# Optimization experiments

Measured on AMD Instinct MI355X. Metric: run time of the kernel, lower is better.

The kernel has to match this reference:

```python
import jax, jax.numpy as jnp
import numpy as np

EMB = 128
SQRT_EMB = 128 ** 0.5
LOGIT_CLIP = 10.0


def setup_inputs() -> dict:
    key = jax.random.key(0)
    ks = jax.random.split(key, 10)
    B, N, M, D = 128, 512, 512, EMB
    s = 1.0 / np.sqrt(D)
    return {
        "encoded_last_node": jax.random.normal(ks[0], (B, N, D), jnp.float32),
        "load": jax.random.uniform(ks[1], (B, N), jnp.float32),
        "cur_dist": jax.random.uniform(ks[2], (B, N, M), jnp.float32),
        "log_scale": jnp.ones((), jnp.float32),
        "ninf_mask": jnp.zeros((B, N, M), jnp.float32),
        "encoded_nodes": jax.random.normal(ks[3], (B, M, D), jnp.float32),
        "Wq_last": jax.random.normal(ks[4], (D, D + 1), jnp.float32) * s,
        "Wk": jax.random.normal(ks[5], (D, D), jnp.float32) * s,
        "Wv": jax.random.normal(ks[6], (D, D), jnp.float32) * s,
        "alpha1": jnp.ones((1,), jnp.float32),
        "alpha2": jnp.ones((1,), jnp.float32),
    }


def reference(encoded_last_node, load, cur_dist, log_scale, ninf_mask,
              encoded_nodes, Wq_last, Wk, Wv, alpha1, alpha2):
    # set_kv
    k = jnp.einsum('bmd,ed->bme', encoded_nodes, Wk)   # (B,M,D)
    v = jnp.einsum('bmd,ed->bme', encoded_nodes, Wv)   # (B,M,D)
    # query from last node + load
    input_cat = jnp.concatenate([encoded_last_node, load[:, :, None]], axis=2)  # (B,N,D+1)
    q = jnp.einsum('bnc,ec->bne', input_cat, Wq_last)  # (B,N,D)
    # AAFM: exp-bias linear attention with sigmoid gate
    adaptation_bias = -alpha1[0] * log_scale * cur_dist + ninf_mask  # (B,N,M)
    eb = jnp.exp(adaptation_bias)
    ek = jnp.exp(k)
    num = jnp.einsum('bnm,bmd->bnd', eb, ek * v)
    den = jnp.einsum('bnm,bmd->bnd', eb, ek)
    weighted = jnp.nan_to_num(num / den)  # mirrors torch nan_to_num correction
    aafm_out = jax.nn.sigmoid(q) * weighted  # (B,N,D)
    # single-head decode score against encoder embeddings
    score = jnp.einsum('bnd,bmd->bnm', aafm_out, encoded_nodes)
    score_scaled = score / SQRT_EMB - alpha2[0] * log_scale * cur_dist
    score_masked = LOGIT_CLIP * jnp.tanh(score_scaled) + ninf_mask
    probs = jax.nn.softmax(score_masked, axis=-1)
    return probs
```

## Files before the change

### kernel.cpp

```cpp
#include <hip/hip_runtime.h>
#include <math.h>

#define B 128
#define N 512
#define M 512
#define D 128

typedef __attribute__((ext_vector_type(8))) short s16x8;
typedef __attribute__((ext_vector_type(4))) short s16x4;
typedef __attribute__((ext_vector_type(4))) float f32x4;

#define MFMA16(a, b, c) __builtin_amdgcn_mfma_f32_16x16x32_bf16(a, b, c, 0, 0, 0)

#define FENCE()   asm volatile("" ::: "memory")
#define VMCNT4()  asm volatile("s_waitcnt vmcnt(4)" ::: "memory")
#define VMCNT8()  asm volatile("s_waitcnt vmcnt(8)" ::: "memory")
#define VMCNT12() asm volatile("s_waitcnt vmcnt(12)" ::: "memory")
#define VMCNT16() asm volatile("s_waitcnt vmcnt(16)" ::: "memory")
#define VMCNT20() asm volatile("s_waitcnt vmcnt(20)" ::: "memory")
#define LGKMCNT0() asm volatile("s_waitcnt lgkmcnt(0)" ::: "memory")
#define SCHEDBAR() __builtin_amdgcn_sched_barrier(0)

__device__ __forceinline__ void gload16(const void* g, void* l) {
    __builtin_amdgcn_global_load_lds(
        (const __attribute__((address_space(1))) unsigned int*)g,
        (__attribute__((address_space(3))) unsigned int*)l, 16, 0, 0);
}

__device__ __forceinline__ float fast_tanh(float x) {
    x = fminf(fmaxf(x, -15.f), 15.f);
    float E = __expf(2.f * x);
    return 1.f - 2.f / (E + 1.f);
}

__device__ __forceinline__ unsigned short bf16rne(float x) {
    unsigned u = __float_as_uint(x);
    return (unsigned short)((u + 0x7FFF + ((u >> 16) & 1)) >> 16);
}

__device__ __forceinline__ void fsplit(float x, short& h, short& l) {
    unsigned u = __float_as_uint(x);
    h = (short)(u >> 16);
    float fh = __uint_as_float(u & 0xffff0000u);
    l = (short)(__float_as_uint(x - fh) >> 16);
}

__device__ __forceinline__ void fsplit8(float4 x0, float4 x1, s16x8& h, s16x8& l) {
    short a, b;
    fsplit(x0.x, a, b); h[0] = a; l[0] = b;
    fsplit(x0.y, a, b); h[1] = a; l[1] = b;
    fsplit(x0.z, a, b); h[2] = a; l[2] = b;
    fsplit(x0.w, a, b); h[3] = a; l[3] = b;
    fsplit(x1.x, a, b); h[4] = a; l[4] = b;
    fsplit(x1.y, a, b); h[5] = a; l[5] = b;
    fsplit(x1.z, a, b); h[6] = a; l[6] = b;
    fsplit(x1.w, a, b); h[7] = a; l[7] = b;
}

__device__ __forceinline__ void ebpack(float4 c0, float4 c1, float4 f0, float4 f1,
                                       float a1ls, s16x8& a) {
    a[0] = (short)bf16rne(__expf(fmaf(-a1ls, c0.x, f0.x)));
    a[1] = (short)bf16rne(__expf(fmaf(-a1ls, c0.y, f0.y)));
    a[2] = (short)bf16rne(__expf(fmaf(-a1ls, c0.z, f0.z)));
    a[3] = (short)bf16rne(__expf(fmaf(-a1ls, c0.w, f0.w)));
    a[4] = (short)bf16rne(__expf(fmaf(-a1ls, c1.x, f1.x)));
    a[5] = (short)bf16rne(__expf(fmaf(-a1ls, c1.y, f1.y)));
    a[6] = (short)bf16rne(__expf(fmaf(-a1ls, c1.z, f1.z)));
    a[7] = (short)bf16rne(__expf(fmaf(-a1ls, c1.w, f1.w)));
}

__global__ void k_prep_w(const float* __restrict__ Wk, const float* __restrict__ Wv,
                         const float* __restrict__ Wq,
                         unsigned short* __restrict__ Wk_hi, unsigned short* __restrict__ Wk_lo,
                         unsigned short* __restrict__ Wv_hi, unsigned short* __restrict__ Wv_lo,
                         unsigned short* __restrict__ Wq_hi, unsigned short* __restrict__ Wq_lo) {
    int i = blockIdx.x * 256 + threadIdx.x;
    short h, l;
    if (i < 16384) {
        fsplit(Wk[i], h, l); Wk_hi[i] = (unsigned short)h; Wk_lo[i] = (unsigned short)l;
    } else if (i < 32768) {
        int j = i - 16384;
        fsplit(Wv[j], h, l); Wv_hi[j] = (unsigned short)h; Wv_lo[j] = (unsigned short)l;
    } else {
        int j = i - 32768; int e = j >> 7, d = j & 127;
        fsplit(Wq[e * 129 + d], h, l); Wq_hi[j] = (unsigned short)h; Wq_lo[j] = (unsigned short)l;
    }
}

__global__ __launch_bounds__(256) void k_kv(const float* __restrict__ enc,
        const unsigned short* __restrict__ Wk_hi, const unsigned short* __restrict__ Wk_lo,
        const unsigned short* __restrict__ Wv_hi, const unsigned short* __restrict__ Wv_lo,
        unsigned short* __restrict__ EKb, unsigned short* __restrict__ EKVb) {
    int b = blockIdx.y;
    int wave = threadIdx.x >> 6, lane = threadIdx.x & 63;
    int row = lane & 15, kg = lane >> 4;
    int m0 = blockIdx.x * 64 + wave * 16;
    f32x4 acc[16];
#pragma unroll
    for (int i = 0; i < 16; i++) acc[i] = (f32x4)0.f;
    const float* ap = enc + ((size_t)b * M + m0 + row) * D + kg * 8;
#pragma unroll
    for (int ks = 0; ks < 4; ks++) {
        float4 x0 = *(const float4*)(ap + ks * 32);
        float4 x1 = *(const float4*)(ap + ks * 32 + 4);
        s16x8 ah, al;
        fsplit8(x0, x1, ah, al);
        int wb = ks * 32 + kg * 8;
#pragma unroll
        for (int ct = 0; ct < 8; ct++) {
            int e = ct * 16 + row;
            s16x8 bh = *(const s16x8*)(Wk_hi + e * D + wb);
            s16x8 bl = *(const s16x8*)(Wk_lo + e * D + wb);
            acc[ct] = MFMA16(ah, bh, acc[ct]);
            acc[ct] = MFMA16(al, bh, acc[ct]);
            acc[ct] = MFMA16(ah, bl, acc[ct]);
            bh = *(const s16x8*)(Wv_hi + e * D + wb);
            bl = *(const s16x8*)(Wv_lo + e * D + wb);
            acc[8 + ct] = MFMA16(ah, bh, acc[8 + ct]);
            acc[8 + ct] = MFMA16(al, bh, acc[8 + ct]);
            acc[8 + ct] = MFMA16(ah, bl, acc[8 + ct]);
        }
    }
#pragma unroll
    for (int ct = 0; ct < 8; ct++) {
        int e = ct * 16 + row;
        s16x4 kb, vb;
#pragma unroll
        for (int r = 0; r < 4; r++) {
            float ek = __expf(acc[ct][r]);
            float ev = ek * acc[8 + ct][r];
            kb[r] = (short)bf16rne(ek);
            vb[r] = (short)bf16rne(ev);
        }
        int m = m0 + kg * 4;
        int chunk = (m & 31) >> 3;
        int p = chunk ^ (e & 3);
        size_t o = ((size_t)b * D + e) * M + (size_t)(m & ~31) + p * 8 + (m & 7);
        *(s16x4*)(EKb + o) = kb;
        *(s16x4*)(EKVb + o) = vb;
    }
}

__global__ void k_encpack(const float* __restrict__ enc, unsigned short* __restrict__ Eb) {
    size_t i = (size_t)blockIdx.x * 256 + threadIdx.x;
    size_t bm = i >> 4;
    int c = (int)(i & 15);
    int m = (int)(bm & 511);
    int p = c ^ (m & 7);
    const float* src = enc + bm * 128 + c * 8;
    float4 x0 = *(const float4*)(src);
    float4 x1 = *(const float4*)(src + 4);
    s16x8 v;
    v[0] = (short)bf16rne(x0.x); v[1] = (short)bf16rne(x0.y);
    v[2] = (short)bf16rne(x0.z); v[3] = (short)bf16rne(x0.w);
    v[4] = (short)bf16rne(x1.x); v[5] = (short)bf16rne(x1.y);
    v[6] = (short)bf16rne(x1.z); v[7] = (short)bf16rne(x1.w);
    *(s16x8*)(Eb + bm * 128 + p * 8) = v;
}

__global__ __launch_bounds__(256, 3) void k_fused(
        const float* __restrict__ encl, const float* __restrict__ loadv,
        const float* __restrict__ Wq,
        const unsigned short* __restrict__ Wq_hi, const unsigned short* __restrict__ Wq_lo,
        const float* __restrict__ cd, const float* __restrict__ ninf,
        const unsigned short* __restrict__ EKVb, const unsigned short* __restrict__ EKb,
        const unsigned short* __restrict__ Eb,
        const float* __restrict__ a1p, const float* __restrict__ a2p,
        const float* __restrict__ lsp, float* __restrict__ out) {
    int o = blockIdx.x;
    int xcd = o & 7, j = o >> 3;
    int b = ((j >> 4) << 3) + xcd;
    int nb = j & 15;
    int n0 = nb * 32;
    int w = threadIdx.x >> 6, lane = threadIdx.x & 63;
    int row = lane & 15, kg = lane >> 4;
    __shared__ __align__(16) char lds[32768];
    float* redm = (float*)lds;
    float* reds = (float*)(lds + 512);
    float a1ls = a1p[0] * lsp[0];
    float a2ls = a2p[0] * lsp[0];
    const float invs = 0.08838834764831845f;
    char* wb = lds + w * 8192;

    f32x4 sqa[2][2];
#pragma unroll
    for (int s = 0; s < 2; s++)
#pragma unroll
        for (int ct = 0; ct < 2; ct++) sqa[s][ct] = (f32x4)0.f;
#pragma unroll
    for (int s = 0; s < 2; s++) {
        const float* ap = encl + ((size_t)b * N + n0 + s * 16 + row) * D + kg * 8;
#pragma unroll
        for (int ks = 0; ks < 4; ks++) {
            float4 x0 = *(const float4*)(ap + ks * 32);
            float4 x1 = *(const float4*)(ap + ks * 32 + 4);
            s16x8 ah, al;
            fsplit8(x0, x1, ah, al);
            int wqo = ks * 32 + kg * 8;
#pragma unroll
            for (int ct = 0; ct < 2; ct++) {
                int e = w * 32 + ct * 16 + row;
                s16x8 bh = *(const s16x8*)(Wq_hi + e * D + wqo);
                s16x8 bl = *(const s16x8*)(Wq_lo + e * D + wqo);
                sqa[s][ct] = MFMA16(ah, bh, sqa[s][ct]);
                sqa[s][ct] = MFMA16(al, bh, sqa[s][ct]);
                sqa[s][ct] = MFMA16(ah, bl, sqa[s][ct]);
            }
        }
    }
    float sqv[2][2][4];
#pragma unroll
    for (int s = 0; s < 2; s++)
#pragma unroll
        for (int ct = 0; ct < 2; ct++) {
            int e = w * 32 + ct * 16 + row;
            float wcol = Wq[e * 129 + 128];
#pragma unroll
            for (int r = 0; r < 4; r++) {
                int n = n0 + s * 16 + kg * 4 + r;
                float q = sqa[s][ct][r] + loadv[(size_t)b * N + n] * wcol;
                sqv[s][ct][r] = 1.f / (1.f + __expf(-q));
            }
        }
    FENCE();

    f32x4 accN[2][2], accD[2][2];
#pragma unroll
    for (int s = 0; s < 2; s++)
#pragma unroll
        for (int i = 0; i < 2; i++) { accN[s][i] = (f32x4)0.f; accD[s][i] = (f32x4)0.f; }
    const char* gEKV = (const char*)EKVb + (size_t)b * D * M * 2;
    const char* gEK  = (const char*)EKb  + (size_t)b * D * M * 2;
    const float* cdp0 = cd + ((size_t)b * N + n0 + row) * M + kg * 8;
    const float* nfp0 = ninf + ((size_t)b * N + n0 + row) * M + kg * 8;
    const float* cdp1 = cdp0 + (size_t)16 * M;
    const float* nfp1 = nfp0 + (size_t)16 * M;

#define STAGE_B(bufptr, mt)                                                      \
    _Pragma("unroll")                                                            \
    for (int jv = 0; jv < 4; jv++) {                                             \
        int arr = jv >> 1;                                                       \
        int rem = (jv & 1) * 64 + lane;                                          \
        const char* gb = arr ? gEK : gEKV;                                       \
        gload16(gb + (size_t)(w * 32 + (rem >> 2)) * 1024 + (size_t)(mt) * 64 +  \
                    (rem & 3) * 16,                                              \
                (char*)(bufptr) + arr * 2048 + rem * 16);                        \
    }

    float4 Ac[2][2][2], Af[2][2][2];
#define LOAD_A(p, mt)                                                            \
    Ac[p][0][0] = *(const float4*)(cdp0 + (mt) * 32);                            \
    Ac[p][0][1] = *(const float4*)(cdp0 + (mt) * 32 + 4);                        \
    Af[p][0][0] = *(const float4*)(nfp0 + (mt) * 32);                            \
    Af[p][0][1] = *(const float4*)(nfp0 + (mt) * 32 + 4);                        \
    Ac[p][1][0] = *(const float4*)(cdp1 + (mt) * 32);                            \
    Ac[p][1][1] = *(const float4*)(cdp1 + (mt) * 32 + 4);                        \
    Af[p][1][0] = *(const float4*)(nfp1 + (mt) * 32);                            \
    Af[p][1][1] = *(const float4*)(nfp1 + (mt) * 32 + 4);

    LOAD_A(0, 0) FENCE();
    STAGE_B(wb, 0) FENCE();
    LOAD_A(1, 1) FENCE();
    STAGE_B(wb + 4096, 1) FENCE();

    int rbB = row * 64 + ((kg ^ (row & 3)) << 4);
#pragma unroll
    for (int mt = 0; mt < 16; mt++) {
        if (mt < 2) { VMCNT12(); } else if (mt < 15) { VMCNT20(); } else { VMCNT8(); }
        SCHEDBAR();
        int p = mt & 1;
        s16x8 a0, a1;
        ebpack(Ac[p][0][0], Ac[p][0][1], Af[p][0][0], Af[p][0][1], a1ls, a0);
        ebpack(Ac[p][1][0], Ac[p][1][1], Af[p][1][0], Af[p][1][1], a1ls, a1);
        const char* L = wb + p * 4096;
#pragma unroll
        for (int ct = 0; ct < 2; ct++) {
            int ro = ct * 1024 + rbB;
            s16x8 bv = *(const s16x8*)(L + ro);
            s16x8 bk = *(const s16x8*)(L + 2048 + ro);
            accN[0][ct] = MFMA16(a0, bv, accN[0][ct]);
            accN[1][ct] = MFMA16(a1, bv, accN[1][ct]);
            accD[0][ct] = MFMA16(a0, bk, accD[0][ct]);
            accD[1][ct] = MFMA16(a1, bk, accD[1][ct]);
        }
        if (mt <= 13) {
            LGKMCNT0();
            SCHEDBAR();
            STAGE_B(wb + p * 4096, mt + 2) FENCE();
            LOAD_A(p, mt + 2) FENCE();
        }
    }

    __syncthreads();
    unsigned short* af = (unsigned short*)lds;
#pragma unroll
    for (int s = 0; s < 2; s++)
#pragma unroll
        for (int ct = 0; ct < 2; ct++) {
            int e = w * 32 + ct * 16 + row;
#pragma unroll
            for (int r = 0; r < 4; r++) {
                int nl = s * 16 + kg * 4 + r;
                float num = accN[s][ct][r], den = accD[s][ct][r];
                float ww = (den != 0.f) ? num / den : 0.f;
                af[nl * 128 + e] = bf16rne(sqv[s][ct][r] * ww);
            }
        }
    __syncthreads();
    s16x8 afr[2][4];
#pragma unroll
    for (int s = 0; s < 2; s++)
#pragma unroll
        for (int es = 0; es < 4; es++)
            afr[s][es] = *(const s16x8*)(af + (s * 16 + row) * 128 + es * 32 + kg * 8);
    __syncthreads();
    FENCE();

    f32x4 acc[2][8];
#pragma unroll
    for (int s = 0; s < 2; s++)
#pragma unroll
        for (int p = 0; p < 8; p++) acc[s][p] = (f32x4)0.f;
    const char* gEb = (const char*)Eb + (size_t)b * M * 256;

#define STAGE_D(bufptr, p)                                                       \
    _Pragma("unroll")                                                            \
    for (int jv = 0; jv < 4; jv++) {                                             \
        int id = jv * 64 + lane;                                                 \
        gload16(gEb + (size_t)(w * 128 + (p) * 16 + (id >> 4)) * 256 + (id & 15) * 16, \
                (char*)(bufptr) + id * 16);                                      \
    }

    STAGE_D(wb, 0) FENCE();
    STAGE_D(wb + 4096, 1) FENCE();

#pragma unroll
    for (int p = 0; p < 8; p++) {
        if (p == 0) { VMCNT4(); } else if (p < 7) { VMCNT20(); } else { VMCNT16(); }
        SCHEDBAR();
        float cdv[2][4], nfv[2][4];
#pragma unroll
        for (int s = 0; s < 2; s++)
#pragma unroll
            for (int r = 0; r < 4; r++) {
                size_t idx = ((size_t)b * N + n0 + s * 16 + kg * 4 + r) * M
                           + (size_t)w * 128 + (size_t)p * 16 + row;
                cdv[s][r] = cd[idx];
                nfv[s][r] = ninf[idx];
            }
        FENCE();
        const char* L = wb + (p & 1) * 4096;
        int sw = row & 7;
#pragma unroll
        for (int es = 0; es < 4; es++) {
            int ph = (4 * es + kg) ^ sw;
            s16x8 bb = *(const s16x8*)(L + row * 256 + ph * 16);
            acc[0][p] = MFMA16(afr[0][es], bb, acc[0][p]);
            acc[1][p] = MFMA16(afr[1][es], bb, acc[1][p]);
        }
        if (p <= 5) {
            LGKMCNT0();
            SCHEDBAR();
            STAGE_D(wb + (p & 1) * 4096, p + 2) FENCE();
        }
#pragma unroll
        for (int s = 0; s < 2; s++)
#pragma unroll
            for (int r = 0; r < 4; r++) {
                acc[s][p][r] = 10.f * fast_tanh(fmaf(acc[s][p][r], invs, -a2ls * cdv[s][r]))
                             + nfv[s][r];
            }
    }

    __syncthreads();
    float mx[2][4], sm[2][4];
#pragma unroll
    for (int s = 0; s < 2; s++)
#pragma unroll
        for (int r = 0; r < 4; r++) {
            float m = acc[s][0][r];
#pragma unroll
            for (int p = 1; p < 8; p++) m = fmaxf(m, acc[s][p][r]);
#pragma unroll
            for (int sh = 1; sh < 16; sh <<= 1) m = fmaxf(m, __shfl_xor(m, sh, 64));
            mx[s][r] = m;
        }
    if (row == 0) {
#pragma unroll
        for (int s = 0; s < 2; s++)
#pragma unroll
            for (int r = 0; r < 4; r++) redm[(s * 16 + kg * 4 + r) * 4 + w] = mx[s][r];
    }
    __syncthreads();
#pragma unroll
    for (int s = 0; s < 2; s++)
#pragma unroll
        for (int r = 0; r < 4; r++) {
            int nl = s * 16 + kg * 4 + r;
            float m = fmaxf(fmaxf(redm[nl * 4 + 0], redm[nl * 4 + 1]),
                            fmaxf(redm[nl * 4 + 2], redm[nl * 4 + 3]));
            float sum = 0.f;
#pragma unroll
            for (int p = 0; p < 8; p++) {
                float e = __expf(acc[s][p][r] - m);
                acc[s][p][r] = e;
                sum += e;
            }
#pragma unroll
            for (int sh = 1; sh < 16; sh <<= 1) sum += __shfl_xor(sum, sh, 64);
            sm[s][r] = sum;
        }
    if (row == 0) {
#pragma unroll
        for (int s = 0; s < 2; s++)
#pragma unroll
            for (int r = 0; r < 4; r++) reds[(s * 16 + kg * 4 + r) * 4 + w] = sm[s][r];
    }
    __syncthreads();
#pragma unroll
    for (int s = 0; s < 2; s++)
#pragma unroll
        for (int r = 0; r < 4; r++) {
            int nl = s * 16 + kg * 4 + r;
            float inv = 1.f / (reds[nl * 4 + 0] + reds[nl * 4 + 1]
                             + reds[nl * 4 + 2] + reds[nl * 4 + 3]);
            size_t ro = ((size_t)b * N + n0 + nl) * M + (size_t)w * 128 + row;
#pragma unroll
            for (int p = 0; p < 8; p++) {
                out[ro + p * 16] = acc[s][p][r] * inv;
            }
        }
}

extern "C" void kernel_launch(void* const* d_in, const int* in_sizes, int n_in,
                              void* d_out, int out_size, void* d_ws, size_t ws_size,
                              hipStream_t stream) {
    const float* encl  = (const float*)d_in[0];
    const float* loadv = (const float*)d_in[1];
    const float* cdist = (const float*)d_in[2];
    const float* ls    = (const float*)d_in[3];
    const float* ninf  = (const float*)d_in[4];
    const float* enc   = (const float*)d_in[5];
    const float* Wq    = (const float*)d_in[6];
    const float* Wk    = (const float*)d_in[7];
    const float* Wv    = (const float*)d_in[8];
    const float* a1    = (const float*)d_in[9];
    const float* a2    = (const float*)d_in[10];
    char* ws = (char*)d_ws;
    unsigned short* EKb     = (unsigned short*)(ws);
    unsigned short* EKVb    = (unsigned short*)(ws + 16777216);
    unsigned short* Eb      = (unsigned short*)(ws + 33554432);
    unsigned short* Wk_hi   = (unsigned short*)(ws + 50331648);
    unsigned short* Wk_lo   = (unsigned short*)(ws + 50331648 + 32768);
    unsigned short* Wv_hi   = (unsigned short*)(ws + 50331648 + 65536);
    unsigned short* Wv_lo   = (unsigned short*)(ws + 50331648 + 98304);
    unsigned short* Wq_hi   = (unsigned short*)(ws + 50331648 + 131072);
    unsigned short* Wq_lo   = (unsigned short*)(ws + 50331648 + 163840);
    float* out = (float*)d_out;

    k_prep_w<<<192, 256, 0, stream>>>(Wk, Wv, Wq, Wk_hi, Wk_lo, Wv_hi, Wv_lo, Wq_hi, Wq_lo);
    k_kv<<<dim3(8, 128), 256, 0, stream>>>(enc, Wk_hi, Wk_lo, Wv_hi, Wv_lo, EKb, EKVb);
    k_encpack<<<4096, 256, 0, stream>>>(enc, Eb);
    k_fused<<<2048, 256, 0, stream>>>(encl, loadv, Wq, Wq_hi, Wq_lo,
                                      cdist, ninf, EKVb, EKb, Eb,
                                      a1, a2, ls, out);
}
```

Before: 333.7 us.

## Fuse encoder bf16 packing into k_kv and load B operands directly to registers

```diff
diff --git a/kernel.cpp b/kernel.cpp
--- a/kernel.cpp
+++ b/kernel.cpp
@@ -11,21 +11,6 @@
 typedef __attribute__((ext_vector_type(4))) float f32x4;
 
 #define MFMA16(a, b, c) __builtin_amdgcn_mfma_f32_16x16x32_bf16(a, b, c, 0, 0, 0)
-
-#define FENCE()   asm volatile("" ::: "memory")
-#define VMCNT4()  asm volatile("s_waitcnt vmcnt(4)" ::: "memory")
-#define VMCNT8()  asm volatile("s_waitcnt vmcnt(8)" ::: "memory")
-#define VMCNT12() asm volatile("s_waitcnt vmcnt(12)" ::: "memory")
-#define VMCNT16() asm volatile("s_waitcnt vmcnt(16)" ::: "memory")
-#define VMCNT20() asm volatile("s_waitcnt vmcnt(20)" ::: "memory")
-#define LGKMCNT0() asm volatile("s_waitcnt lgkmcnt(0)" ::: "memory")
-#define SCHEDBAR() __builtin_amdgcn_sched_barrier(0)
-
-__device__ __forceinline__ void gload16(const void* g, void* l) {
-    __builtin_amdgcn_global_load_lds(
-        (const __attribute__((address_space(1))) unsigned int*)g,
-        (__attribute__((address_space(3))) unsigned int*)l, 16, 0, 0);
-}
 
 __device__ __forceinline__ float fast_tanh(float x) {
     x = fminf(fmaxf(x, -15.f), 15.f);
@@ -90,7 +75,8 @@
 __global__ __launch_bounds__(256) void k_kv(const float* __restrict__ enc,
         const unsigned short* __restrict__ Wk_hi, const unsigned short* __restrict__ Wk_lo,
         const unsigned short* __restrict__ Wv_hi, const unsigned short* __restrict__ Wv_lo,
-        unsigned short* __restrict__ EKb, unsigned short* __restrict__ EKVb) {
+        unsigned short* __restrict__ EKb, unsigned short* __restrict__ EKVb,
+        unsigned short* __restrict__ Eb) {
     int b = blockIdx.y;
     int wave = threadIdx.x >> 6, lane = threadIdx.x & 63;
     int row = lane & 15, kg = lane >> 4;
@@ -99,12 +85,20 @@
 #pragma unroll
     for (int i = 0; i < 16; i++) acc[i] = (f32x4)0.f;
     const float* ap = enc + ((size_t)b * M + m0 + row) * D + kg * 8;
+    int menc = m0 + row;
 #pragma unroll
     for (int ks = 0; ks < 4; ks++) {
         float4 x0 = *(const float4*)(ap + ks * 32);
         float4 x1 = *(const float4*)(ap + ks * 32 + 4);
         s16x8 ah, al;
         fsplit8(x0, x1, ah, al);
+        s16x8 ev;
+        ev[0] = (short)bf16rne(x0.x); ev[1] = (short)bf16rne(x0.y);
+        ev[2] = (short)bf16rne(x0.z); ev[3] = (short)bf16rne(x0.w);
+        ev[4] = (short)bf16rne(x1.x); ev[5] = (short)bf16rne(x1.y);
+        ev[6] = (short)bf16rne(x1.z); ev[7] = (short)bf16rne(x1.w);
+        int c = ks * 4 + kg;
+        *(s16x8*)(Eb + ((size_t)b * M + menc) * D + (size_t)((c ^ (menc & 7)) * 8)) = ev;
         int wb = ks * 32 + kg * 8;
 #pragma unroll
         for (int ct = 0; ct < 8; ct++) {
@@ -139,23 +133,6 @@
         *(s16x4*)(EKb + o) = kb;
         *(s16x4*)(EKVb + o) = vb;
     }
-}
-
-__global__ void k_encpack(const float* __restrict__ enc, unsigned short* __restrict__ Eb) {
-    size_t i = (size_t)blockIdx.x * 256 + threadIdx.x;
-    size_t bm = i >> 4;
-    int c = (int)(i & 15);
-    int m = (int)(bm & 511);
-    int p = c ^ (m & 7);
-    const float* src = enc + bm * 128 + c * 8;
-    float4 x0 = *(const float4*)(src);
-    float4 x1 = *(const float4*)(src + 4);
-    s16x8 v;
-    v[0] = (short)bf16rne(x0.x); v[1] = (short)bf16rne(x0.y);
-    v[2] = (short)bf16rne(x0.z); v[3] = (short)bf16rne(x0.w);
-    v[4] = (short)bf16rne(x1.x); v[5] = (short)bf16rne(x1.y);
-    v[6] = (short)bf16rne(x1.z); v[7] = (short)bf16rne(x1.w);
-    *(s16x8*)(Eb + bm * 128 + p * 8) = v;
 }
 
 __global__ __launch_bounds__(256, 3) void k_fused(
@@ -174,13 +151,11 @@
     int n0 = nb * 32;
     int w = threadIdx.x >> 6, lane = threadIdx.x & 63;
     int row = lane & 15, kg = lane >> 4;
-    __shared__ __align__(16) char lds[32768];
-    float* redm = (float*)lds;
-    float* reds = (float*)(lds + 512);
+    __shared__ __align__(16) unsigned short af[32 * 128];
+    __shared__ float redm[32][4], reds[32][4];
     float a1ls = a1p[0] * lsp[0];
     float a2ls = a2p[0] * lsp[0];
     const float invs = 0.08838834764831845f;
-    char* wb = lds + w * 8192;
 
     f32x4 sqa[2][2];
 #pragma unroll
@@ -222,32 +197,26 @@
                 sqv[s][ct][r] = 1.f / (1.f + __expf(-q));
             }
         }
-    FENCE();
 
     f32x4 accN[2][2], accD[2][2];
 #pragma unroll
     for (int s = 0; s < 2; s++)
 #pragma unroll
         for (int i = 0; i < 2; i++) { accN[s][i] = (f32x4)0.f; accD[s][i] = (f32x4)0.f; }
-    const char* gEKV = (const char*)EKVb + (size_t)b * D * M * 2;
-    const char* gEK  = (const char*)EKb  + (size_t)b * D * M * 2;
     const float* cdp0 = cd + ((size_t)b * N + n0 + row) * M + kg * 8;
     const float* nfp0 = ninf + ((size_t)b * N + n0 + row) * M + kg * 8;
     const float* cdp1 = cdp0 + (size_t)16 * M;
     const float* nfp1 = nfp0 + (size_t)16 * M;
-
-#define STAGE_B(bufptr, mt)                                                      \
-    _Pragma("unroll")                                                            \
-    for (int jv = 0; jv < 4; jv++) {                                             \
-        int arr = jv >> 1;                                                       \
-        int rem = (jv & 1) * 64 + lane;                                          \
-        const char* gb = arr ? gEK : gEKV;                                       \
-        gload16(gb + (size_t)(w * 32 + (rem >> 2)) * 1024 + (size_t)(mt) * 64 +  \
-                    (rem & 3) * 16,                                              \
-                (char*)(bufptr) + arr * 2048 + rem * 16);                        \
-    }
-
+    int swo = (kg ^ (row & 3)) << 4;
+    const char* bV[2]; const char* bK[2];
+#pragma unroll
+    for (int ct = 0; ct < 2; ct++) {
+        int e = w * 32 + ct * 16 + row;
+        bV[ct] = (const char*)EKVb + (((size_t)b * D + e) * M) * 2 + swo;
+        bK[ct] = (const char*)EKb  + (((size_t)b * D + e) * M) * 2 + swo;
+    }
     float4 Ac[2][2][2], Af[2][2][2];
+    s16x8 BV[2][2], BK[2][2];
 #define LOAD_A(p, mt)                                                            \
     Ac[p][0][0] = *(const float4*)(cdp0 + (mt) * 32);                            \
     Ac[p][0][1] = *(const float4*)(cdp0 + (mt) * 32 + 4);                        \
@@ -257,42 +226,34 @@
     Ac[p][1][1] = *(const float4*)(cdp1 + (mt) * 32 + 4);                        \
     Af[p][1][0] = *(const float4*)(nfp1 + (mt) * 32);                            \
     Af[p][1][1] = *(const float4*)(nfp1 + (mt) * 32 + 4);
-
-    LOAD_A(0, 0) FENCE();
-    STAGE_B(wb, 0) FENCE();
-    LOAD_A(1, 1) FENCE();
-    STAGE_B(wb + 4096, 1) FENCE();
-
-    int rbB = row * 64 + ((kg ^ (row & 3)) << 4);
+#define LOAD_B(p, mt)                                                            \
+    BV[p][0] = *(const s16x8*)(bV[0] + (mt) * 64);                               \
+    BV[p][1] = *(const s16x8*)(bV[1] + (mt) * 64);                               \
+    BK[p][0] = *(const s16x8*)(bK[0] + (mt) * 64);                               \
+    BK[p][1] = *(const s16x8*)(bK[1] + (mt) * 64);
+
+    LOAD_A(0, 0) LOAD_B(0, 0)
+    LOAD_A(1, 1) LOAD_B(1, 1)
+
 #pragma unroll
     for (int mt = 0; mt < 16; mt++) {
-        if (mt < 2) { VMCNT12(); } else if (mt < 15) { VMCNT20(); } else { VMCNT8(); }
-        SCHEDBAR();
         int p = mt & 1;
         s16x8 a0, a1;
         ebpack(Ac[p][0][0], Ac[p][0][1], Af[p][0][0], Af[p][0][1], a1ls, a0);
         ebpack(Ac[p][1][0], Ac[p][1][1], Af[p][1][0], Af[p][1][1], a1ls, a1);
-        const char* L = wb + p * 4096;
 #pragma unroll
         for (int ct = 0; ct < 2; ct++) {
-            int ro = ct * 1024 + rbB;
-            s16x8 bv = *(const s16x8*)(L + ro);
-            s16x8 bk = *(const s16x8*)(L + 2048 + ro);
-            accN[0][ct] = MFMA16(a0, bv, accN[0][ct]);
-            accN[1][ct] = MFMA16(a1, bv, accN[1][ct]);
-            accD[0][ct] = MFMA16(a0, bk, accD[0][ct]);
-            accD[1][ct] = MFMA16(a1, bk, accD[1][ct]);
+            accN[0][ct] = MFMA16(a0, BV[p][ct], accN[0][ct]);
+            accN[1][ct] = MFMA16(a1, BV[p][ct], accN[1][ct]);
+            accD[0][ct] = MFMA16(a0, BK[p][ct], accD[0][ct]);
+            accD[1][ct] = MFMA16(a1, BK[p][ct], accD[1][ct]);
         }
         if (mt <= 13) {
-            LGKMCNT0();
-            SCHEDBAR();
-            STAGE_B(wb + p * 4096, mt + 2) FENCE();
-            LOAD_A(p, mt + 2) FENCE();
-        }
-    }
-
-    __syncthreads();
-    unsigned short* af = (unsigned short*)lds;
+            LOAD_A(p, mt + 2)
+            LOAD_B(p, mt + 2)
+        }
+    }
+
 #pragma unroll
     for (int s = 0; s < 2; s++)
 #pragma unroll
@@ -313,66 +274,56 @@
 #pragma unroll
         for (int es = 0; es < 4; es++)
             afr[s][es] = *(const s16x8*)(af + (s * 16 + row) * 128 + es * 32 + kg * 8);
-    __syncthreads();
-    FENCE();
 
     f32x4 acc[2][8];
 #pragma unroll
     for (int s = 0; s < 2; s++)
 #pragma unroll
         for (int p = 0; p < 8; p++) acc[s][p] = (f32x4)0.f;
-    const char* gEb = (const char*)Eb + (size_t)b * M * 256;
-
-#define STAGE_D(bufptr, p)                                                       \
+    int dsw = row & 7;
+    const char* bE = (const char*)Eb + ((size_t)b * M + w * 128 + row) * 256;
+    const float* cdD0 = cd + ((size_t)b * N + n0 + kg * 4) * M + w * 128 + row;
+    const float* nfD0 = ninf + ((size_t)b * N + n0 + kg * 4) * M + w * 128 + row;
+    const float* cdD1 = cdD0 + (size_t)16 * M;
+    const float* nfD1 = nfD0 + (size_t)16 * M;
+    s16x8 EF[2][4];
+    float cdv[2][2][4], nfv[2][2][4];
+#define LOAD_E(p, pt)                                                            \
+    EF[p][0] = *(const s16x8*)(bE + (size_t)(pt) * 4096 + ((0 + kg) ^ dsw) * 16);  \
+    EF[p][1] = *(const s16x8*)(bE + (size_t)(pt) * 4096 + ((4 + kg) ^ dsw) * 16);  \
+    EF[p][2] = *(const s16x8*)(bE + (size_t)(pt) * 4096 + ((8 + kg) ^ dsw) * 16);  \
+    EF[p][3] = *(const s16x8*)(bE + (size_t)(pt) * 4096 + ((12 + kg) ^ dsw) * 16);
+#define LOAD_CDNF(sl, pt)                                                        \
     _Pragma("unroll")                                                            \
-    for (int jv = 0; jv < 4; jv++) {                                             \
-        int id = jv * 64 + lane;                                                 \
-        gload16(gEb + (size_t)(w * 128 + (p) * 16 + (id >> 4)) * 256 + (id & 15) * 16, \
-                (char*)(bufptr) + id * 16);                                      \
-    }
-
-    STAGE_D(wb, 0) FENCE();
-    STAGE_D(wb + 4096, 1) FENCE();
+    for (int r = 0; r < 4; r++) {                                                \
+        cdv[sl][0][r] = cdD0[(size_t)r * M + (pt) * 16];                         \
+        nfv[sl][0][r] = nfD0[(size_t)r * M + (pt) * 16];                         \
+        cdv[sl][1][r] = cdD1[(size_t)r * M + (pt) * 16];                         \
+        nfv[sl][1][r] = nfD1[(size_t)r * M + (pt) * 16];                         \
+    }
+
+    LOAD_E(0, 0) LOAD_E(1, 1)
+    LOAD_CDNF(0, 0)
 
 #pragma unroll
     for (int p = 0; p < 8; p++) {
-        if (p == 0) { VMCNT4(); } else if (p < 7) { VMCNT20(); } else { VMCNT16(); }
-        SCHEDBAR();
-        float cdv[2][4], nfv[2][4];
+        int par = p & 1;
+#pragma unroll
+        for (int es = 0; es < 4; es++) {
+            acc[0][p] = MFMA16(afr[0][es], EF[par][es], acc[0][p]);
+            acc[1][p] = MFMA16(afr[1][es], EF[par][es], acc[1][p]);
+        }
+        if (p <= 5) { LOAD_E(par, p + 2) }
+        if (p <= 6) { LOAD_CDNF(par ^ 1, p + 1) }
 #pragma unroll
         for (int s = 0; s < 2; s++)
 #pragma unroll
             for (int r = 0; r < 4; r++) {
-                size_t idx = ((size_t)b * N + n0 + s * 16 + kg * 4 + r) * M
-                           + (size_t)w * 128 + (size_t)p * 16 + row;
-                cdv[s][r] = cd[idx];
-                nfv[s][r] = ninf[idx];
-            }
-        FENCE();
-        const char* L = wb + (p & 1) * 4096;
-        int sw = row & 7;
-#pragma unroll
-        for (int es = 0; es < 4; es++) {
-            int ph = (4 * es + kg) ^ sw;
-            s16x8 bb = *(const s16x8*)(L + row * 256 + ph * 16);
-            acc[0][p] = MFMA16(afr[0][es], bb, acc[0][p]);
-            acc[1][p] = MFMA16(afr[1][es], bb, acc[1][p]);
-        }
-        if (p <= 5) {
-            LGKMCNT0();
-            SCHEDBAR();
-            STAGE_D(wb + (p & 1) * 4096, p + 2) FENCE();
-        }
-#pragma unroll
-        for (int s = 0; s < 2; s++)
-#pragma unroll
-            for (int r = 0; r < 4; r++) {
-                acc[s][p][r] = 10.f * fast_tanh(fmaf(acc[s][p][r], invs, -a2ls * cdv[s][r]))
-                             + nfv[s][r];
-            }
-    }
-
-    __syncthreads();
+                acc[s][p][r] = 10.f * fast_tanh(fmaf(acc[s][p][r], invs, -a2ls * cdv[par][s][r]))
+                             + nfv[par][s][r];
+            }
+    }
+
     float mx[2][4], sm[2][4];
 #pragma unroll
     for (int s = 0; s < 2; s++)
@@ -389,7 +340,7 @@
 #pragma unroll
         for (int s = 0; s < 2; s++)
 #pragma unroll
-            for (int r = 0; r < 4; r++) redm[(s * 16 + kg * 4 + r) * 4 + w] = mx[s][r];
+            for (int r = 0; r < 4; r++) redm[s * 16 + kg * 4 + r][w] = mx[s][r];
     }
     __syncthreads();
 #pragma unroll
@@ -397,8 +348,8 @@
 #pragma unroll
         for (int r = 0; r < 4; r++) {
             int nl = s * 16 + kg * 4 + r;
-            float m = fmaxf(fmaxf(redm[nl * 4 + 0], redm[nl * 4 + 1]),
-                            fmaxf(redm[nl * 4 + 2], redm[nl * 4 + 3]));
+            float m = fmaxf(fmaxf(redm[nl][0], redm[nl][1]),
+                            fmaxf(redm[nl][2], redm[nl][3]));
             float sum = 0.f;
 #pragma unroll
             for (int p = 0; p < 8; p++) {
@@ -414,7 +365,7 @@
 #pragma unroll
         for (int s = 0; s < 2; s++)
 #pragma unroll
-            for (int r = 0; r < 4; r++) reds[(s * 16 + kg * 4 + r) * 4 + w] = sm[s][r];
+            for (int r = 0; r < 4; r++) reds[s * 16 + kg * 4 + r][w] = sm[s][r];
     }
     __syncthreads();
 #pragma unroll
@@ -422,8 +373,7 @@
 #pragma unroll
         for (int r = 0; r < 4; r++) {
             int nl = s * 16 + kg * 4 + r;
-            float inv = 1.f / (reds[nl * 4 + 0] + reds[nl * 4 + 1]
-                             + reds[nl * 4 + 2] + reds[nl * 4 + 3]);
+            float inv = 1.f / (reds[nl][0] + reds[nl][1] + reds[nl][2] + reds[nl][3]);
             size_t ro = ((size_t)b * N + n0 + nl) * M + (size_t)w * 128 + row;
 #pragma unroll
             for (int p = 0; p < 8; p++) {
@@ -459,8 +409,7 @@
     float* out = (float*)d_out;
 
     k_prep_w<<<192, 256, 0, stream>>>(Wk, Wv, Wq, Wk_hi, Wk_lo, Wv_hi, Wv_lo, Wq_hi, Wq_lo);
-    k_kv<<<dim3(8, 128), 256, 0, stream>>>(enc, Wk_hi, Wk_lo, Wv_hi, Wv_lo, EKb, EKVb);
-    k_encpack<<<4096, 256, 0, stream>>>(enc, Eb);
+    k_kv<<<dim3(8, 128), 256, 0, stream>>>(enc, Wk_hi, Wk_lo, Wv_hi, Wv_lo, EKb, EKVb, Eb);
     k_fused<<<2048, 256, 0, stream>>>(encl, loadv, Wq, Wq_hi, Wq_lo,
                                       cdist, ninf, EKVb, EKb, Eb,
                                       a1, a2, ls, out);
```

Result: no change. 329.2 us (-1.4%).
